# Kernel tuning notes

Measured on AMD Instinct MI355X. Metric: run time of the kernel, lower is better.

The kernel has to match this reference:

```python
import jax, jax.numpy as jnp
import numpy as np

HIDDEN = 3584
N_HEADS = 16
N_KV = 8
HEAD_DIM = 256
INTER = 14336
EPS = 1e-6
SCALING = 256.0 ** -0.5  # query_pre_attn_scalar ** -0.5
SOFTCAP = 50.0
WINDOW = 1024
B, S = 2, 2048


def rmsnorm(x, w, eps=EPS):
    # Gemma2 style: scale by (1 + weight), weight zero-initialized
    var = jnp.mean(x * x, axis=-1, keepdims=True)
    return x * jax.lax.rsqrt(var + eps) * (1.0 + w)


def rotate_half(x):
    half = x.shape[-1] // 2
    return jnp.concatenate([-x[..., half:], x[..., :half]], axis=-1)


def setup_inputs() -> dict:
    key = jax.random.key(0)
    ks = jax.random.split(key, 12)
    hidden_states = jax.random.normal(ks[0], (B, S, HIDDEN), jnp.float32)
    # RoPE tables (theta = 10000)
    inv_freq = 1.0 / (10000.0 ** (np.arange(0, HEAD_DIM, 2, dtype=np.float32) / HEAD_DIM))
    t = np.arange(S, dtype=np.float32)
    freqs = np.outer(t, inv_freq)  # [S, HEAD_DIM/2]
    emb = np.concatenate([freqs, freqs], axis=-1)  # [S, HEAD_DIM]
    cos = jnp.asarray(np.cos(emb))
    sin = jnp.asarray(np.sin(emb))
    sd = lambda fan_in: 1.0 / np.sqrt(fan_in)
    Wq = jax.random.normal(ks[1], (N_HEADS * HEAD_DIM, HIDDEN), jnp.float32) * sd(HIDDEN)
    Wk = jax.random.normal(ks[2], (N_KV * HEAD_DIM, HIDDEN), jnp.float32) * sd(HIDDEN)
    Wv = jax.random.normal(ks[3], (N_KV * HEAD_DIM, HIDDEN), jnp.float32) * sd(HIDDEN)
    Wo = jax.random.normal(ks[4], (HIDDEN, N_HEADS * HEAD_DIM), jnp.float32) * sd(N_HEADS * HEAD_DIM)
    Wgate = jax.random.normal(ks[5], (INTER, HIDDEN), jnp.float32) * sd(HIDDEN)
    Wup = jax.random.normal(ks[6], (INTER, HIDDEN), jnp.float32) * sd(HIDDEN)
    Wdown = jax.random.normal(ks[7], (HIDDEN, INTER), jnp.float32) * sd(INTER)
    # RMSNorm weights zero-init per Gemma2 (effective scale 1.0), small perturbation
    w_in_ln = jax.random.normal(ks[8], (HIDDEN,), jnp.float32) * 0.02
    w_post_attn_ln = jax.random.normal(ks[9], (HIDDEN,), jnp.float32) * 0.02
    w_pre_ff_ln = jax.random.normal(ks[10], (HIDDEN,), jnp.float32) * 0.02
    w_post_ff_ln = jax.random.normal(ks[11], (HIDDEN,), jnp.float32) * 0.02
    return dict(hidden_states=hidden_states, cos=cos, sin=sin, Wq=Wq, Wk=Wk, Wv=Wv,
                Wo=Wo, Wgate=Wgate, Wup=Wup, Wdown=Wdown, w_in_ln=w_in_ln,
                w_post_attn_ln=w_post_attn_ln, w_pre_ff_ln=w_pre_ff_ln,
                w_post_ff_ln=w_post_ff_ln)


def _decoder_layer(hidden_states, cos, sin, Wq, Wk, Wv, Wo, Wgate, Wup, Wdown,
                   w_in_ln, w_post_attn_ln, w_pre_ff_ln, w_post_ff_ln):
    b, s, _ = hidden_states.shape
    residual = hidden_states
    x = rmsnorm(hidden_states, w_in_ln)

    # QKV projections (bias=False), bsnd layout
    q = jnp.einsum('bsh,oh->bso', x, Wq).reshape(b, s, N_HEADS, HEAD_DIM)
    k = jnp.einsum('bsh,oh->bso', x, Wk).reshape(b, s, N_KV, HEAD_DIM)
    v = jnp.einsum('bsh,oh->bso', x, Wv).reshape(b, s, N_KV, HEAD_DIM)

    # RoPE with explicit cos/sin, half-rotation; broadcast over batch & heads
    c = cos[None, :, None, :]
    sn = sin[None, :, None, :]
    q = q * c + rotate_half(q) * sn
    k = k * c + rotate_half(k) * sn

    # GQA: repeat KV heads
    rep = N_HEADS // N_KV
    k = jnp.repeat(k, rep, axis=2)  # [b, s, H, D]
    v = jnp.repeat(v, rep, axis=2)

    # scores with custom scaling + tanh softcap
    scores = jnp.einsum('bqhd,bkhd->bhqk', q, k) * SCALING
    scores = SOFTCAP * jnp.tanh(scores / SOFTCAP)

    # causal + sliding-window mask: attend to j with i-WINDOW < j <= i
    i = jnp.arange(s)[:, None]
    j = jnp.arange(s)[None, :]
    allowed = (j <= i) & (j > i - WINDOW)
    scores = jnp.where(allowed[None, None], scores, jnp.float32(-1e30))

    probs = jax.nn.softmax(scores, axis=-1)
    attn = jnp.einsum('bhqk,bkhd->bqhd', probs, v).reshape(b, s, N_HEADS * HEAD_DIM)
    attn = jnp.einsum('bso,ho->bsh', attn, Wo)

    hidden_states = residual + rmsnorm(attn, w_post_attn_ln)

    residual = hidden_states
    y = rmsnorm(hidden_states, w_pre_ff_ln)
    gate = jax.nn.gelu(jnp.einsum('bsh,ih->bsi', y, Wgate), approximate=True)
    up = jnp.einsum('bsh,ih->bsi', y, Wup)
    mlp = jnp.einsum('bsi,hi->bsh', gate * up, Wdown)
    hidden_states = residual + rmsnorm(mlp, w_post_ff_ln)
    return hidden_states


def reference(hidden_states, cos, sin, Wq, Wk, Wv, Wo, Wgate, Wup, Wdown,
              w_in_ln, w_post_attn_ln, w_pre_ff_ln, w_post_ff_ln):
    return _decoder_layer(hidden_states, cos, sin, Wq, Wk, Wv, Wo, Wgate, Wup,
                          Wdown, w_in_ln, w_post_attn_ln, w_pre_ff_ln, w_post_ff_ln)
```

## Files before the change

### kernel.cpp

```cpp
#include <hip/hip_runtime.h>
#include <hip/hip_bf16.h>

typedef __hip_bfloat16 bf16;
typedef __bf16 bf16x8_t __attribute__((ext_vector_type(8)));
typedef float f32x4_t __attribute__((ext_vector_type(4)));
typedef unsigned short u16x8_t __attribute__((ext_vector_type(8)));

#define HID 3584
#define SEQ 2048
#define NBATCH 2
#define MTOK 4096
#define NHEADS 16
#define NKVH 8
#define HDIM 256
#define QOUT 4096
#define KOUT 2048
#define INTERD 14336
#define EPSF 1e-6f

static __device__ __forceinline__ unsigned short f2bu(float f) {
  union { bf16 b; unsigned short u; } cv;
  cv.b = __float2bfloat16(f);
  return cv.u;
}

static __device__ __forceinline__ f32x4_t mfma16(bf16x8_t a, bf16x8_t b, f32x4_t c) {
  return __builtin_amdgcn_mfma_f32_16x16x32_bf16(a, b, c, 0, 0, 0);
}

static __device__ __forceinline__ void gl_lds16(const void* g, void* l) {
  __builtin_amdgcn_global_load_lds((__attribute__((address_space(1))) void*)g,
                                   (__attribute__((address_space(3))) void*)l,
                                   16, 0, 0);
}

static __device__ __forceinline__ float block_reduce_sum(float v) {
  __shared__ float buf[4];
  #pragma unroll
  for (int m = 1; m < 64; m <<= 1) v += __shfl_xor(v, m, 64);
  __syncthreads();
  if ((threadIdx.x & 63) == 0) buf[threadIdx.x >> 6] = v;
  __syncthreads();
  return buf[0] + buf[1] + buf[2] + buf[3];
}

__global__ __launch_bounds__(256) void cvt_w(
    const float* __restrict__ src, bf16* __restrict__ dst, int n) {
  const int stride = gridDim.x * 256 * 8;
  for (int i = (blockIdx.x * 256 + threadIdx.x) * 8; i < n; i += stride) {
    const float4 a = *(const float4*)(src + i);
    const float4 b = *(const float4*)(src + i + 4);
    u16x8_t o;
    o[0] = f2bu(a.x); o[1] = f2bu(a.y); o[2] = f2bu(a.z); o[3] = f2bu(a.w);
    o[4] = f2bu(b.x); o[5] = f2bu(b.y); o[6] = f2bu(b.z); o[7] = f2bu(b.w);
    *(u16x8_t*)(dst + i) = o;
  }
}

enum { EPI_BF16 = 0, EPI_F32 = 1, EPI_GELUMUL = 2, EPI_QK = 3, EPI_VSW = 4 };

template <int EPI>
__global__ __launch_bounds__(256, 3) void gemm4w(
    const bf16* __restrict__ A, const bf16* __restrict__ Bw,
    void* __restrict__ Cout, const bf16* __restrict__ aux,
    void* __restrict__ C2, int Ndim, int Kdim, int mshift) {
  __shared__ __align__(16) char L[32768];

  const int NT = Kdim >> 5;
  const int NB = gridDim.x;
  const int bid = blockIdx.x;
  const int sw = (bid & 7) * (NB >> 3) + (bid >> 3);
  const int m0 = (sw & ((1 << mshift) - 1)) << 7;
  const int n0 = (sw >> mshift) << 7;

  const int tid = threadIdx.x;
  const int wid = tid >> 6, l = tid & 63;
  const int wm = wid >> 1, wn = wid & 1;
  const int lr = l & 15, lg = l >> 4;

  const int rl = tid >> 2;
  const int lc8 = (((l & 3) ^ ((l >> 3) & 3)) << 3);
  const bf16* srcA = A + (size_t)(m0 + rl) * Kdim + lc8;
  const bf16* srcB = Bw + (size_t)(n0 + rl) * Kdim + lc8;
  const size_t K64 = (size_t)Kdim << 6;

  auto STAGE2 = [&](int op, int tl) {
    if (tl >= NT) return;
    const bf16* s = (op ? srcB : srcA) + ((size_t)tl << 5);
    char* d = L + ((tl & 1) << 14) + (op << 13) + (wid << 10);
    gl_lds16(s, d);
    gl_lds16(s + K64, d + 4096);
  };

  const int arow = wm * 64 + lr;
  const int brow = wn * 64 + lr;
  const int ch = (lg ^ ((lr >> 1) & 3)) << 4;
  auto LDA = [&](int mi, int c) {
    return *(const bf16x8_t*)(L + (c << 14) + (arow + mi * 16) * 64 + ch);
  };
  auto LDB = [&](int ni, int c) {
    return *(const bf16x8_t*)(L + (c << 14) + 8192 + (brow + ni * 16) * 64 + ch);
  };

  f32x4_t acc[4][4];
  #pragma unroll
  for (int i = 0; i < 4; i++)
    #pragma unroll
    for (int j = 0; j < 4; j++) acc[i][j] = (f32x4_t){0.f, 0.f, 0.f, 0.f};

  bf16x8_t fa[4], fb[4];

  STAGE2(1, 0); STAGE2(0, 0); STAGE2(1, 1); STAGE2(0, 1);
  asm volatile("s_waitcnt vmcnt(4)" ::: "memory");

#define TILE(T, C)                                                             \
  {                                                                            \
    __builtin_amdgcn_s_barrier();                          \
    _Pragma("unroll") for (int mi = 0; mi < 4; ++mi) fa[mi] = LDA(mi, (C));    \
    _Pragma("unroll") for (int ni = 0; ni < 4; ++ni) fb[ni] = LDB(ni, (C));    \
    asm volatile("s_waitcnt lgkmcnt(0)" ::: "memory");                         \
    __builtin_amdgcn_s_barrier();          \
    STAGE2(1, (T) + 2);                                                        \
    STAGE2(0, (T) + 2);                                                        \
    __builtin_amdgcn_s_setprio(1);                                             \
    _Pragma("unroll") for (int mi = 0; mi < 4; ++mi)                           \
    _Pragma("unroll") for (int ni = 0; ni < 4; ++ni)                           \
      acc[mi][ni] = mfma16(fa[mi], fb[ni], acc[mi][ni]);                       \
    __builtin_amdgcn_s_setprio(0);                                             \
    if ((T) + 2 < NT) {                                                        \
      asm volatile("s_waitcnt vmcnt(4)" ::: "memory");                         \
    } else {                                                                   \
      asm volatile("s_waitcnt vmcnt(0)" ::: "memory");                         \
    }                                                                          \
  }

  for (int t = 0; t < NT; t += 2) {
    TILE(t, 0);
    TILE(t + 1, 1);
  }
#undef TILE

  const int row0 = m0 + wm * 64 + lg * 4;
  const int col0 = n0 + wn * 64 + lr;
  #pragma unroll
  for (int mi = 0; mi < 4; mi++) {
    #pragma unroll
    for (int ni = 0; ni < 4; ni++) {
      #pragma unroll
      for (int r = 0; r < 4; r++) {
        const int row = row0 + mi * 16 + r;
        const int col = col0 + ni * 16;
        const float v = acc[mi][ni][r];
        if constexpr (EPI == EPI_BF16) {
          ((bf16*)Cout)[(size_t)row * Ndim + col] = __float2bfloat16(v);
        } else if constexpr (EPI == EPI_F32) {
          ((float*)Cout)[(size_t)row * Ndim + col] = v;
        } else if constexpr (EPI == EPI_QK) {
          if (col < 4096) {
            ((bf16*)Cout)[(size_t)row * 4096 + col] = __float2bfloat16(v);
          } else {
            ((bf16*)C2)[(size_t)row * 2048 + (col - 4096)] =
                __float2bfloat16(v);
          }
        } else if constexpr (EPI == EPI_VSW) {
          const int bb = col >> 11, s = col & 2047;
          ((bf16*)Cout)[(((size_t)((bb * 8 + (row >> 8)) * 256 + (row & 255)))
                         << 11) + s] = __float2bfloat16(v);
        } else {
          const float g = __bfloat162float(aux[(size_t)row * Ndim + col]);
          const float u = 0.7978845608028654f * (g + 0.044715f * g * g * g);
          const float gl = 0.5f * g * (1.f + tanhf(u));
          ((bf16*)Cout)[(size_t)row * Ndim + col] = __float2bfloat16(gl * v);
        }
      }
    }
  }
  (void)aux; (void)C2;
}

__global__ __launch_bounds__(256) void rmsnorm_in(
    const float* __restrict__ x, const float* __restrict__ w,
    bf16* __restrict__ out) {
  const int row = blockIdx.x, t = threadIdx.x;
  const float4* xr = (const float4*)(x + (size_t)row * HID);
  float4 v[4];
  float ss = 0.f;
  #pragma unroll
  for (int j = 0; j < 4; j++) {
    const int idx = t + 256 * j;
    if (idx < HID / 4) {
      v[j] = xr[idx];
      ss += v[j].x * v[j].x + v[j].y * v[j].y + v[j].z * v[j].z + v[j].w * v[j].w;
    }
  }
  ss = block_reduce_sum(ss);
  const float sc = rsqrtf(ss * (1.f / HID) + EPSF);
  const float4* w4 = (const float4*)w;
  bf16* orow = out + (size_t)row * HID;
  #pragma unroll
  for (int j = 0; j < 4; j++) {
    const int idx = t + 256 * j;
    if (idx < HID / 4) {
      const float4 wv = w4[idx];
      ushort4 o;
      o.x = f2bu(v[j].x * sc * (1.f + wv.x));
      o.y = f2bu(v[j].y * sc * (1.f + wv.y));
      o.z = f2bu(v[j].z * sc * (1.f + wv.z));
      o.w = f2bu(v[j].w * sc * (1.f + wv.w));
      *(ushort4*)(orow + idx * 4) = o;
    }
  }
}

__global__ __launch_bounds__(128) void rope_kernel(
    bf16* __restrict__ q, bf16* __restrict__ k,
    const float* __restrict__ cosb, const float* __restrict__ sinb) {
  const int tok = blockIdx.x;
  const int hs = blockIdx.y;
  const int d = threadIdx.x;
  const int s = tok & (SEQ - 1);
  bf16* ptr = (hs < NHEADS)
                  ? q + (size_t)tok * QOUT + hs * HDIM
                  : k + (size_t)tok * KOUT + (hs - NHEADS) * HDIM;
  const float c = cosb[s * HDIM + d];
  const float sn = sinb[s * HDIM + d];
  const float x0 = __bfloat162float(ptr[d]);
  const float x1 = __bfloat162float(ptr[d + 128]);
  ptr[d] = __float2bfloat16(x0 * c - x1 * sn);
  ptr[d + 128] = __float2bfloat16(x1 * c + x0 * sn);
}

__global__ __launch_bounds__(256) void attn_kernel(
    const bf16* __restrict__ q, const bf16* __restrict__ k,
    const bf16* __restrict__ vt, bf16* __restrict__ out) {
  __shared__ __align__(16) bf16 plds[4][16 * 32];

  const int qt = blockIdx.x, h = blockIdx.y, b = blockIdx.z;
  const int w = threadIdx.x >> 6, l = threadIdx.x & 63;
  const int kvh = h >> 1;
  const int qbase = qt * 64 + w * 16;
  const int lr = l & 15, lg = l >> 4, lk = lg * 8;

  bf16x8_t qf[8];
  const bf16* qrow = q + (size_t)(b * SEQ + qbase + lr) * QOUT + h * HDIM;
  #pragma unroll
  for (int c = 0; c < 8; c++) qf[c] = *(const bf16x8_t*)(qrow + c * 32 + lk);

  f32x4_t acc[16];
  #pragma unroll
  for (int i = 0; i < 16; i++) acc[i] = (f32x4_t){0.f, 0.f, 0.f, 0.f};
  float L[4] = {0.f, 0.f, 0.f, 0.f};

  const bf16* kp = k + (size_t)(b * SEQ) * KOUT + kvh * HDIM;
  const bf16* vp = vt + (size_t)(b * NKVH + kvh) * HDIM * SEQ;
  bf16* pl = &plds[w][0];

  int kstart = qbase - 1023;
  if (kstart < 0) kstart = 0;
  kstart &= ~31;
  const int kend = qbase + 15;

  for (int kb = kstart; kb <= kend; kb += 32) {
    f32x4_t s0 = (f32x4_t){0.f, 0.f, 0.f, 0.f};
    f32x4_t s1 = (f32x4_t){0.f, 0.f, 0.f, 0.f};
    #pragma unroll
    for (int c = 0; c < 8; c++) {
      bf16x8_t k0 = *(const bf16x8_t*)(kp + (size_t)(kb + lr) * KOUT + c * 32 + lk);
      bf16x8_t k1 = *(const bf16x8_t*)(kp + (size_t)(kb + 16 + lr) * KOUT + c * 32 + lk);
      s0 = mfma16(qf[c], k0, s0);
      s1 = mfma16(qf[c], k1, s1);
    }
    float p[8];
    #pragma unroll
    for (int sub = 0; sub < 2; sub++) {
      const int j = kb + sub * 16 + lr;
      #pragma unroll
      for (int r = 0; r < 4; r++) {
        const int i = qbase + lg * 4 + r;
        float sc = (sub ? s1[r] : s0[r]) * 0.0625f;
        sc = 50.f * tanhf(sc * 0.02f);
        const bool ok = (j <= i) && (j > i - 1024);
        p[sub * 4 + r] = ok ? __expf(sc) : 0.f;
      }
    }
    #pragma unroll
    for (int r = 0; r < 4; r++) {
      float ps = p[r] + p[4 + r];
      ps += __shfl_xor(ps, 1, 64);
      ps += __shfl_xor(ps, 2, 64);
      ps += __shfl_xor(ps, 4, 64);
      ps += __shfl_xor(ps, 8, 64);
      L[r] += ps;
    }
    #pragma unroll
    for (int sub = 0; sub < 2; sub++)
      #pragma unroll
      for (int r = 0; r < 4; r++)
        pl[(lg * 4 + r) * 32 + sub * 16 + lr] = __float2bfloat16(p[sub * 4 + r]);
    asm volatile("s_waitcnt lgkmcnt(0)" ::: "memory");
    const bf16x8_t pa = *(const bf16x8_t*)(pl + lr * 32 + lk);
    #pragma unroll
    for (int dt = 0; dt < 16; dt++) {
      bf16x8_t bv = *(const bf16x8_t*)(vp + (size_t)(dt * 16 + lr) * SEQ + kb + lk);
      acc[dt] = mfma16(pa, bv, acc[dt]);
    }
  }

  float rL[4];
  #pragma unroll
  for (int r = 0; r < 4; r++) rL[r] = 1.f / L[r];
  #pragma unroll
  for (int dt = 0; dt < 16; dt++) {
    #pragma unroll
    for (int r = 0; r < 4; r++) {
      const int tok = b * SEQ + qbase + lg * 4 + r;
      out[(size_t)tok * QOUT + h * HDIM + dt * 16 + lr] =
          __float2bfloat16(acc[dt][r] * rL[r]);
    }
  }
}

__global__ __launch_bounds__(256) void fuse_attn(
    const float* __restrict__ hidden, const float* __restrict__ ap,
    const float* __restrict__ w_post, const float* __restrict__ w_pre,
    float* __restrict__ h1, bf16* __restrict__ y) {
  const int row = blockIdx.x, t = threadIdx.x;
  const float4* ar = (const float4*)(ap + (size_t)row * HID);
  const float4* hr = (const float4*)(hidden + (size_t)row * HID);
  float4 a[4];
  float ss = 0.f;
  #pragma unroll
  for (int j = 0; j < 4; j++) {
    const int idx = t + 256 * j;
    if (idx < HID / 4) {
      a[j] = ar[idx];
      ss += a[j].x * a[j].x + a[j].y * a[j].y + a[j].z * a[j].z + a[j].w * a[j].w;
    }
  }
  ss = block_reduce_sum(ss);
  const float sc = rsqrtf(ss * (1.f / HID) + EPSF);
  const float4* wpo = (const float4*)w_post;
  float4* h1r = (float4*)(h1 + (size_t)row * HID);
  float4 hv[4];
  float ss2 = 0.f;
  #pragma unroll
  for (int j = 0; j < 4; j++) {
    const int idx = t + 256 * j;
    if (idx < HID / 4) {
      const float4 wv = wpo[idx];
      const float4 x = hr[idx];
      hv[j].x = x.x + a[j].x * sc * (1.f + wv.x);
      hv[j].y = x.y + a[j].y * sc * (1.f + wv.y);
      hv[j].z = x.z + a[j].z * sc * (1.f + wv.z);
      hv[j].w = x.w + a[j].w * sc * (1.f + wv.w);
      ss2 += hv[j].x * hv[j].x + hv[j].y * hv[j].y + hv[j].z * hv[j].z + hv[j].w * hv[j].w;
      h1r[idx] = hv[j];
    }
  }
  ss2 = block_reduce_sum(ss2);
  const float sc2 = rsqrtf(ss2 * (1.f / HID) + EPSF);
  const float4* wpr = (const float4*)w_pre;
  bf16* yr = y + (size_t)row * HID;
  #pragma unroll
  for (int j = 0; j < 4; j++) {
    const int idx = t + 256 * j;
    if (idx < HID / 4) {
      const float4 wv = wpr[idx];
      ushort4 o;
      o.x = f2bu(hv[j].x * sc2 * (1.f + wv.x));
      o.y = f2bu(hv[j].y * sc2 * (1.f + wv.y));
      o.z = f2bu(hv[j].z * sc2 * (1.f + wv.z));
      o.w = f2bu(hv[j].w * sc2 * (1.f + wv.w));
      *(ushort4*)(yr + idx * 4) = o;
    }
  }
}

__global__ __launch_bounds__(256) void fuse_out(
    const float* __restrict__ h1, const float* __restrict__ mlp,
    const float* __restrict__ w, float* __restrict__ out) {
  const int row = blockIdx.x, t = threadIdx.x;
  const float4* mr = (const float4*)(mlp + (size_t)row * HID);
  float4 m[4];
  float ss = 0.f;
  #pragma unroll
  for (int j = 0; j < 4; j++) {
    const int idx = t + 256 * j;
    if (idx < HID / 4) {
      m[j] = mr[idx];
      ss += m[j].x * m[j].x + m[j].y * m[j].y + m[j].z * m[j].z + m[j].w * m[j].w;
    }
  }
  ss = block_reduce_sum(ss);
  const float sc = rsqrtf(ss * (1.f / HID) + EPSF);
  const float4* hr = (const float4*)(h1 + (size_t)row * HID);
  const float4* w4 = (const float4*)w;
  float4* orow = (float4*)(out + (size_t)row * HID);
  #pragma unroll
  for (int j = 0; j < 4; j++) {
    const int idx = t + 256 * j;
    if (idx < HID / 4) {
      const float4 wv = w4[idx];
      const float4 x = hr[idx];
      float4 o;
      o.x = x.x + m[j].x * sc * (1.f + wv.x);
      o.y = x.y + m[j].y * sc * (1.f + wv.y);
      o.z = x.z + m[j].z * sc * (1.f + wv.z);
      o.w = x.w + m[j].w * sc * (1.f + wv.w);
      orow[idx] = o;
    }
  }
}

extern "C" void kernel_launch(void* const* d_in, const int* in_sizes, int n_in,
                              void* d_out, int out_size, void* d_ws,
                              size_t ws_size, hipStream_t stream) {
  const float* hidden = (const float*)d_in[0];
  const float* cosb = (const float*)d_in[1];
  const float* sinb = (const float*)d_in[2];
  const float* Wq = (const float*)d_in[3];
  const float* Wk = (const float*)d_in[4];
  const float* Wv = (const float*)d_in[5];
  const float* Wo = (const float*)d_in[6];
  const float* Wgate = (const float*)d_in[7];
  const float* Wup = (const float*)d_in[8];
  const float* Wdown = (const float*)d_in[9];
  const float* w_in = (const float*)d_in[10];
  const float* w_post_attn = (const float*)d_in[11];
  const float* w_pre_ff = (const float*)d_in[12];
  const float* w_post_ff = (const float*)d_in[13];
  float* out = (float*)d_out;

  (void)in_sizes; (void)n_in; (void)out_size; (void)ws_size;

  const size_t WB = 102760448;
  char* ws = (char*)d_ws;
  bf16* wbuf = (bf16*)ws;
  char* ab = ws + WB;

  bf16* xn = (bf16*)(ab);
  bf16* q = (bf16*)(ab + 29360128);
  float* attn_proj = (float*)(ab);
  float* mlp = (float*)(ab);
  bf16* kbuf = (bf16*)(ab + 62914560);
  bf16* vt = (bf16*)(ab + 62914560 + 16777216);
  bf16* attn_out = (bf16*)(ab + 62914560 + 33554432);
  float* h1 = (float*)(ab + 62914560);
  bf16* y = (bf16*)(ab + 130023424);
  bf16* gate = (bf16*)(ab + 159383552);

  rmsnorm_in<<<MTOK, 256, 0, stream>>>(hidden, w_in, xn);

  cvt_w<<<4096, 256, 0, stream>>>(Wq, wbuf, QOUT * HID);
  cvt_w<<<2048, 256, 0, stream>>>(Wk, wbuf + (size_t)QOUT * HID, KOUT * HID);
  cvt_w<<<2048, 256, 0, stream>>>(Wv, wbuf + (size_t)(QOUT + KOUT) * HID,
                                  KOUT * HID);
  gemm4w<EPI_QK><<<(6144 / 128) * 32, 256, 0, stream>>>(
      xn, wbuf, q, nullptr, kbuf, 6144, HID, 5);
  gemm4w<EPI_VSW><<<(4096 / 128) * 16, 256, 0, stream>>>(
      wbuf + (size_t)(QOUT + KOUT) * HID, xn, vt, nullptr, nullptr,
      4096, HID, 4);
  rope_kernel<<<dim3(MTOK, NHEADS + NKVH), 128, 0, stream>>>(q, kbuf, cosb, sinb);
  attn_kernel<<<dim3(SEQ / 64, NHEADS, NBATCH), 256, 0, stream>>>(
      q, kbuf, vt, attn_out);
  cvt_w<<<4096, 256, 0, stream>>>(Wo, wbuf, HID * QOUT);
  gemm4w<EPI_F32><<<(HID / 128) * 32, 256, 0, stream>>>(
      attn_out, wbuf, attn_proj, nullptr, nullptr, HID, QOUT, 5);
  fuse_attn<<<MTOK, 256, 0, stream>>>(hidden, attn_proj, w_post_attn,
                                      w_pre_ff, h1, y);
  cvt_w<<<4096, 256, 0, stream>>>(Wgate, wbuf, INTERD * HID);
  gemm4w<EPI_BF16><<<(INTERD / 128) * 32, 256, 0, stream>>>(
      y, wbuf, gate, nullptr, nullptr, INTERD, HID, 5);
  cvt_w<<<4096, 256, 0, stream>>>(Wup, wbuf, INTERD * HID);
  gemm4w<EPI_GELUMUL><<<(INTERD / 128) * 32, 256, 0, stream>>>(
      y, wbuf, gate, gate, nullptr, INTERD, HID, 5);
  cvt_w<<<4096, 256, 0, stream>>>(Wdown, wbuf, INTERD * HID);
  gemm4w<EPI_F32><<<(HID / 128) * 32, 256, 0, stream>>>(
      gate, wbuf, mlp, nullptr, nullptr, HID, INTERD, 5);

  fuse_out<<<MTOK, 256, 0, stream>>>(h1, mlp, w_post_ff, out);
}
```

Baseline: 3.218 ms.

## Replace pipelined 16x16 MFMA GEMM with single-buffered 32x32x16 MFMA GEMM

Swaps the GEMM kernel for a version using 32x32x16 bf16 MFMA instructions with a 2x2 accumulator tile per wave. This reduces LDS fragment reads per flop. The double-buffered global-to-LDS prefetch, the blockIdx swizzle for cache locality and the launch-bounds occupancy hint are removed in favour of a simple 2D grid with two barriers per K step. This risks exposing memory latency that the old pipeline hid.

```diff
diff --git a/kernel.cpp b/kernel.cpp
--- a/kernel.cpp
+++ b/kernel.cpp
@@ -4,6 +4,7 @@
 typedef __hip_bfloat16 bf16;
 typedef __bf16 bf16x8_t __attribute__((ext_vector_type(8)));
 typedef float f32x4_t __attribute__((ext_vector_type(4)));
+typedef float f32x16_t __attribute__((ext_vector_type(16)));
 typedef unsigned short u16x8_t __attribute__((ext_vector_type(8)));
 
 #define HID 3584
@@ -28,6 +29,10 @@
   return __builtin_amdgcn_mfma_f32_16x16x32_bf16(a, b, c, 0, 0, 0);
 }
 
+static __device__ __forceinline__ f32x16_t mfma32(bf16x8_t a, bf16x8_t b, f32x16_t c) {
+  return __builtin_amdgcn_mfma_f32_32x32x16_bf16(a, b, c, 0, 0, 0);
+}
+
 static __device__ __forceinline__ void gl_lds16(const void* g, void* l) {
   __builtin_amdgcn_global_load_lds((__attribute__((address_space(1))) void*)g,
                                    (__attribute__((address_space(3))) void*)l,
@@ -60,97 +65,67 @@
 enum { EPI_BF16 = 0, EPI_F32 = 1, EPI_GELUMUL = 2, EPI_QK = 3, EPI_VSW = 4 };
 
 template <int EPI>
-__global__ __launch_bounds__(256, 3) void gemm4w(
+__global__ __launch_bounds__(256) void gemm32(
     const bf16* __restrict__ A, const bf16* __restrict__ Bw,
     void* __restrict__ Cout, const bf16* __restrict__ aux,
-    void* __restrict__ C2, int Ndim, int Kdim, int mshift) {
-  __shared__ __align__(16) char L[32768];
-
-  const int NT = Kdim >> 5;
-  const int NB = gridDim.x;
-  const int bid = blockIdx.x;
-  const int sw = (bid & 7) * (NB >> 3) + (bid >> 3);
-  const int m0 = (sw & ((1 << mshift) - 1)) << 7;
-  const int n0 = (sw >> mshift) << 7;
-
-  const int tid = threadIdx.x;
-  const int wid = tid >> 6, l = tid & 63;
+    void* __restrict__ C2, int Ndim, int Kdim) {
+  __shared__ __align__(16) bf16 As[128 * 32];
+  __shared__ __align__(16) bf16 Bs[128 * 32];
+
+  const int n0 = blockIdx.x * 128;
+  const int m0 = blockIdx.y * 128;
+  const int t = threadIdx.x;
+  const int wid = t >> 6, l = t & 63;
   const int wm = wid >> 1, wn = wid & 1;
-  const int lr = l & 15, lg = l >> 4;
-
-  const int rl = tid >> 2;
-  const int lc8 = (((l & 3) ^ ((l >> 3) & 3)) << 3);
-  const bf16* srcA = A + (size_t)(m0 + rl) * Kdim + lc8;
-  const bf16* srcB = Bw + (size_t)(n0 + rl) * Kdim + lc8;
-  const size_t K64 = (size_t)Kdim << 6;
-
-  auto STAGE2 = [&](int op, int tl) {
-    if (tl >= NT) return;
-    const bf16* s = (op ? srcB : srcA) + ((size_t)tl << 5);
-    char* d = L + ((tl & 1) << 14) + (op << 13) + (wid << 10);
-    gl_lds16(s, d);
-    gl_lds16(s + K64, d + 4096);
-  };
-
-  const int arow = wm * 64 + lr;
-  const int brow = wn * 64 + lr;
-  const int ch = (lg ^ ((lr >> 1) & 3)) << 4;
-  auto LDA = [&](int mi, int c) {
-    return *(const bf16x8_t*)(L + (c << 14) + (arow + mi * 16) * 64 + ch);
-  };
-  auto LDB = [&](int ni, int c) {
-    return *(const bf16x8_t*)(L + (c << 14) + 8192 + (brow + ni * 16) * 64 + ch);
-  };
-
-  f32x4_t acc[4][4];
-  #pragma unroll
-  for (int i = 0; i < 4; i++)
-    #pragma unroll
-    for (int j = 0; j < 4; j++) acc[i][j] = (f32x4_t){0.f, 0.f, 0.f, 0.f};
-
-  bf16x8_t fa[4], fb[4];
-
-  STAGE2(1, 0); STAGE2(0, 0); STAGE2(1, 1); STAGE2(0, 1);
-  asm volatile("s_waitcnt vmcnt(4)" ::: "memory");
-
-#define TILE(T, C)                                                             \
-  {                                                                            \
-    __builtin_amdgcn_s_barrier();                          \
-    _Pragma("unroll") for (int mi = 0; mi < 4; ++mi) fa[mi] = LDA(mi, (C));    \
-    _Pragma("unroll") for (int ni = 0; ni < 4; ++ni) fb[ni] = LDB(ni, (C));    \
-    asm volatile("s_waitcnt lgkmcnt(0)" ::: "memory");                         \
-    __builtin_amdgcn_s_barrier();          \
-    STAGE2(1, (T) + 2);                                                        \
-    STAGE2(0, (T) + 2);                                                        \
-    __builtin_amdgcn_s_setprio(1);                                             \
-    _Pragma("unroll") for (int mi = 0; mi < 4; ++mi)                           \
-    _Pragma("unroll") for (int ni = 0; ni < 4; ++ni)                           \
-      acc[mi][ni] = mfma16(fa[mi], fb[ni], acc[mi][ni]);                       \
-    __builtin_amdgcn_s_setprio(0);                                             \
-    if ((T) + 2 < NT) {                                                        \
-      asm volatile("s_waitcnt vmcnt(4)" ::: "memory");                         \
-    } else {                                                                   \
-      asm volatile("s_waitcnt vmcnt(0)" ::: "memory");                         \
-    }                                                                          \
-  }
-
-  for (int t = 0; t < NT; t += 2) {
-    TILE(t, 0);
-    TILE(t + 1, 1);
-  }
-#undef TILE
-
-  const int row0 = m0 + wm * 64 + lg * 4;
-  const int col0 = n0 + wn * 64 + lr;
-  #pragma unroll
-  for (int mi = 0; mi < 4; mi++) {
-    #pragma unroll
-    for (int ni = 0; ni < 4; ni++) {
+  const int lc = l & 31, lh = l >> 5;
+
+  const int rS = t >> 2;
+  const int cS = (((t & 3) ^ ((t >> 4) & 3)) << 3);
+  const bf16* Ab0 = A + (size_t)(m0 + rS) * Kdim + cS;
+  const bf16* Ab1 = A + (size_t)(m0 + rS + 64) * Kdim + cS;
+  const bf16* Bb0 = Bw + (size_t)(n0 + rS) * Kdim + cS;
+  const bf16* Bb1 = Bw + (size_t)(n0 + rS + 64) * Kdim + cS;
+
+  f32x16_t zz = {};
+  f32x16_t acc[2][2] = {{zz, zz}, {zz, zz}};
+
+  const int rsw = (lc >> 2) & 3;
+  const int arow0 = (wm * 64 + lc) * 32;
+  const int brow0 = (wn * 64 + lc) * 32;
+
+  for (int kt = 0; kt < Kdim; kt += 32) {
+    __syncthreads();
+    gl_lds16(Ab0 + kt, (char*)As + t * 16);
+    gl_lds16(Ab1 + kt, (char*)As + 4096 + t * 16);
+    gl_lds16(Bb0 + kt, (char*)Bs + t * 16);
+    gl_lds16(Bb1 + kt, (char*)Bs + 4096 + t * 16);
+    __syncthreads();
+
+    #pragma unroll
+    for (int kc = 0; kc < 2; kc++) {
+      const int ch = (((kc << 1) + lh) ^ rsw) << 3;
+      bf16x8_t fa0 = *(const bf16x8_t*)(As + arow0 + ch);
+      bf16x8_t fa1 = *(const bf16x8_t*)(As + arow0 + 32 * 32 + ch);
+      bf16x8_t fb0 = *(const bf16x8_t*)(Bs + brow0 + ch);
+      bf16x8_t fb1 = *(const bf16x8_t*)(Bs + brow0 + 32 * 32 + ch);
+      acc[0][0] = mfma32(fa0, fb0, acc[0][0]);
+      acc[0][1] = mfma32(fa0, fb1, acc[0][1]);
+      acc[1][0] = mfma32(fa1, fb0, acc[1][0]);
+      acc[1][1] = mfma32(fa1, fb1, acc[1][1]);
+    }
+  }
+
+  const int colb = n0 + wn * 64 + lc;
+  const int rowb = m0 + wm * 64 + 4 * lh;
+  #pragma unroll
+  for (int mi = 0; mi < 2; mi++) {
+    #pragma unroll
+    for (int ni = 0; ni < 2; ni++) {
       #pragma unroll
-      for (int r = 0; r < 4; r++) {
-        const int row = row0 + mi * 16 + r;
-        const int col = col0 + ni * 16;
-        const float v = acc[mi][ni][r];
+      for (int reg = 0; reg < 16; reg++) {
+        const int row = rowb + mi * 32 + (reg & 3) + 8 * (reg >> 2);
+        const int col = colb + ni * 32;
+        const float v = acc[mi][ni][reg];
         if constexpr (EPI == EPI_BF16) {
           ((bf16*)Cout)[(size_t)row * Ndim + col] = __float2bfloat16(v);
         } else if constexpr (EPI == EPI_F32) {
@@ -455,28 +430,28 @@
   cvt_w<<<2048, 256, 0, stream>>>(Wk, wbuf + (size_t)QOUT * HID, KOUT * HID);
   cvt_w<<<2048, 256, 0, stream>>>(Wv, wbuf + (size_t)(QOUT + KOUT) * HID,
                                   KOUT * HID);
-  gemm4w<EPI_QK><<<(6144 / 128) * 32, 256, 0, stream>>>(
-      xn, wbuf, q, nullptr, kbuf, 6144, HID, 5);
-  gemm4w<EPI_VSW><<<(4096 / 128) * 16, 256, 0, stream>>>(
+  gemm32<EPI_QK><<<dim3(6144 / 128, MTOK / 128), 256, 0, stream>>>(
+      xn, wbuf, q, nullptr, kbuf, 6144, HID);
+  gemm32<EPI_VSW><<<dim3(MTOK / 128, KOUT / 128), 256, 0, stream>>>(
       wbuf + (size_t)(QOUT + KOUT) * HID, xn, vt, nullptr, nullptr,
-      4096, HID, 4);
+      MTOK, HID);
   rope_kernel<<<dim3(MTOK, NHEADS + NKVH), 128, 0, stream>>>(q, kbuf, cosb, sinb);
   attn_kernel<<<dim3(SEQ / 64, NHEADS, NBATCH), 256, 0, stream>>>(
       q, kbuf, vt, attn_out);
   cvt_w<<<4096, 256, 0, stream>>>(Wo, wbuf, HID * QOUT);
-  gemm4w<EPI_F32><<<(HID / 128) * 32, 256, 0, stream>>>(
-      attn_out, wbuf, attn_proj, nullptr, nullptr, HID, QOUT, 5);
+  gemm32<EPI_F32><<<dim3(HID / 128, MTOK / 128), 256, 0, stream>>>(
+      attn_out, wbuf, attn_proj, nullptr, nullptr, HID, QOUT);
   fuse_attn<<<MTOK, 256, 0, stream>>>(hidden, attn_proj, w_post_attn,
                                       w_pre_ff, h1, y);
   cvt_w<<<4096, 256, 0, stream>>>(Wgate, wbuf, INTERD * HID);
-  gemm4w<EPI_BF16><<<(INTERD / 128) * 32, 256, 0, stream>>>(
-      y, wbuf, gate, nullptr, nullptr, INTERD, HID, 5);
+  gemm32<EPI_BF16><<<dim3(INTERD / 128, MTOK / 128), 256, 0, stream>>>(
+      y, wbuf, gate, nullptr, nullptr, INTERD, HID);
   cvt_w<<<4096, 256, 0, stream>>>(Wup, wbuf, INTERD * HID);
-  gemm4w<EPI_GELUMUL><<<(INTERD / 128) * 32, 256, 0, stream>>>(
-      y, wbuf, gate, gate, nullptr, INTERD, HID, 5);
+  gemm32<EPI_GELUMUL><<<dim3(INTERD / 128, MTOK / 128), 256, 0, stream>>>(
+      y, wbuf, gate, gate, nullptr, INTERD, HID);
   cvt_w<<<4096, 256, 0, stream>>>(Wdown, wbuf, INTERD * HID);
-  gemm4w<EPI_F32><<<(HID / 128) * 32, 256, 0, stream>>>(
-      gate, wbuf, mlp, nullptr, nullptr, HID, INTERD, 5);
+  gemm32<EPI_F32><<<dim3(HID / 128, MTOK / 128), 256, 0, stream>>>(
+      gate, wbuf, mlp, nullptr, nullptr, HID, INTERD);
 
   fuse_out<<<MTOK, 256, 0, stream>>>(h1, mlp, w_post_ff, out);
 }
```

Result: no change. 3.266 ms (+1.5%).
